# Kernel tuning notes

Measured on AMD Instinct MI355X. Metric: run time of the kernel, lower is better.

The kernel has to match this reference:

```python
import jax, jax.numpy as jnp
import numpy as np

CHUNK = 32  # config.scan_chunk_size


def setup_inputs() -> dict:
    key = jax.random.key(0)
    ks = jax.random.split(key, 12)
    B, T, D, SD, OD = 8, 2048, 512, 256, 64
    w = lambda i, shape: (jax.random.normal(ks[i], shape, dtype=jnp.float32) * 0.02)
    return {
        "x": jax.random.normal(ks[0], (B, T, D), dtype=jnp.float32),
        "gate_W": w(1, (D, SD)), "gate_b": jnp.zeros((SD,), jnp.float32),
        "in_W": w(2, (D, SD)), "in_b": jnp.zeros((SD,), jnp.float32),
        "out_W": w(3, (SD, D)), "out_b": jnp.zeros((D,), jnp.float32),
        "opv_W": w(4, (D, OD)), "opv_b": jnp.zeros((OD,), jnp.float32),
        "opk_W": w(5, (D, OD)), "opk_b": jnp.zeros((OD,), jnp.float32),
        "opq_W": w(6, (D, OD)), "opq_b": jnp.zeros((OD,), jnp.float32),
        "op_decay": jnp.full((OD,), 0.95, jnp.float32),
        "opout_W": w(7, (OD, D)), "opout_b": jnp.zeros((D,), jnp.float32),
        "ln_g": jnp.ones((D,), jnp.float32), "ln_b": jnp.zeros((D,), jnp.float32),
    }


def _chunked_scan(gates, drive, K):
    # gates, drive: [B,T,SD]; T divisible by K
    B, T, SD = drive.shape
    nC = T // K
    a = gates.reshape(B, nC, K, SD)
    b = drive.reshape(B, nC, K, SD)
    log_cum_a = jnp.cumsum(jnp.log(jnp.maximum(a, 1e-6)), axis=2)
    cum_a = jnp.exp(log_cum_a)                               # [B,nC,K,SD]
    cum_wb = jnp.cumsum(b / jnp.maximum(cum_a, 1e-8), axis=2)
    # sequential scan over chunks to propagate the carry h
    def step(h, inputs):
        ca_last, wb_last = inputs                            # [B,SD] each
        h_new = ca_last * (h + wb_last)
        return h_new, h                                      # emit h BEFORE this chunk
    h0 = jnp.zeros((B, SD), drive.dtype)
    _, h_prev = jax.lax.scan(
        step, h0,
        (cum_a[:, :, -1].transpose(1, 0, 2), cum_wb[:, :, -1].transpose(1, 0, 2)))
    h_prev = h_prev.transpose(1, 0, 2)                       # [B,nC,SD]
    states = cum_a * (h_prev[:, :, None, :] + cum_wb)
    return states.reshape(B, T, SD)


def _binding_scan_outer(v, k, q, decay):
    # v,k,q: [B,T,OD]; S_t = diag(decay) @ S_{t-1} + v_t k_t^T; o_t = S_t q_t
    B, T, OD = v.shape
    def step(S, vkq):
        vt, kt, qt = vkq                                     # [B,OD] each
        S_new = decay[None, :, None] * S + vt[:, :, None] * kt[:, None, :]
        o = jnp.einsum('bij,bj->bi', S_new, qt)
        return S_new, o
    S0 = jnp.zeros((B, OD, OD), v.dtype)
    _, outs = jax.lax.scan(step, S0, (v.transpose(1, 0, 2), k.transpose(1, 0, 2), q.transpose(1, 0, 2)))
    return outs.transpose(1, 0, 2)                           # [B,T,OD]


def reference(x, gate_W, gate_b, in_W, in_b, out_W, out_b,
              opv_W, opv_b, opk_W, opk_b, opq_W, opq_b, op_decay,
              opout_W, opout_b, ln_g, ln_b):
    gates = jax.nn.sigmoid(x @ gate_W + gate_b)              # [B,T,SD]
    drive = (1.0 - gates) * (x @ in_W + in_b)
    states = _chunked_scan(gates, drive, CHUNK)
    scan_out = states @ out_W + out_b                        # [B,T,D]
    # binding scan (mode='outer')
    v = x @ opv_W + opv_b
    k = x @ opk_W + opk_b
    q = x @ opq_W + opq_b
    dec = jax.nn.sigmoid(op_decay)
    bind = _binding_scan_outer(v, k, q, dec) @ opout_W + opout_b
    y = x + scan_out + bind
    mu = jnp.mean(y, axis=-1, keepdims=True)
    var = jnp.mean((y - mu) ** 2, axis=-1, keepdims=True)
    return (y - mu) / jnp.sqrt(var + 1e-5) * ln_g + ln_b
```

## Files before the change

kernel.cpp:

```cpp
#include <hip/hip_runtime.h>
#include <hip/hip_bf16.h>
#include <hip/hip_fp16.h>
#include <math.h>

#define BB 8
#define TT 2048
#define DD 512
#define SD 256
#define OD 64
#define CHUNK 32
#define NC 64
#define CB 64
#define NCB 32
#define MM (BB*TT)
#define KCAT 320

typedef __attribute__((ext_vector_type(8))) short bf16x8_t;
typedef __attribute__((ext_vector_type(4))) float f32x4;

__device__ __forceinline__ void gload_lds16(const void* gsrc, void* ldst) {
    __builtin_amdgcn_global_load_lds(
        (const __attribute__((address_space(1))) unsigned int*)gsrc,
        (__attribute__((address_space(3))) unsigned int*)ldst,
        16, 0, 0);
}

__device__ __forceinline__ float4 ldh4(const __half* p) {
    __half2 a = *(const __half2*)p;
    __half2 b = *(const __half2*)(p + 2);
    float2 fa = __half22float2(a), fb = __half22float2(b);
    return make_float4(fa.x, fa.y, fb.x, fb.y);
}

__global__ __launch_bounds__(256) void conv_w(
    const float* __restrict__ gate_W, const float* __restrict__ gate_b,
    const float* __restrict__ in_W,   const float* __restrict__ in_b,
    const float* __restrict__ opv_W,  const float* __restrict__ opk_W,
    const float* __restrict__ opq_W,
    const float* __restrict__ opv_b,  const float* __restrict__ opk_b,
    const float* __restrict__ opq_b,
    const float* __restrict__ out_W,  const float* __restrict__ out_b,
    const float* __restrict__ opout_W, const float* __restrict__ opout_b,
    __hip_bfloat16* __restrict__ Wcat,  __hip_bfloat16* __restrict__ Wcomb,
    float* __restrict__ bias_cat, float* __restrict__ bias_comb)
{
    int idx = blockIdx.x * 256 + threadIdx.x;
    if (idx < 393216) {
        int n = idx >> 9, k = idx & 511;
        float v;
        if (n < 256)       v = gate_W[k * 256 + n];
        else if (n < 512)  v = in_W[k * 256 + (n - 256)];
        else if (n < 704) {
            int h = (n - 512) >> 6, j = (n - 512) & 63;
            const float* W = (h == 0) ? opv_W : (h == 1) ? opk_W : opq_W;
            v = W[k * 64 + j];
        } else v = 0.f;
        Wcat[idx] = __float2bfloat16(v);
        return;
    }
    idx -= 393216;
    if (idx < 163840) {
        int n = idx / KCAT, k = idx % KCAT;
        float v = (k < 256) ? out_W[k * 512 + n] : opout_W[(k - 256) * 512 + n];
        Wcomb[idx] = __float2bfloat16(v);
        return;
    }
    idx -= 163840;
    if (idx < 768) {
        float v;
        if (idx < 256)      v = gate_b[idx];
        else if (idx < 512) v = in_b[idx - 256];
        else if (idx < 704) {
            int h = (idx - 512) >> 6, j = (idx - 512) & 63;
            v = (h == 0) ? opv_b[j] : (h == 1) ? opk_b[j] : opq_b[j];
        } else v = 0.f;
        bias_cat[idx] = v;
        return;
    }
    idx -= 768;
    if (idx < 512) bias_comb[idx] = out_b[idx] + opout_b[idx];
}

__global__ __launch_bounds__(512, 6) void gemm_proj(
    const float* __restrict__ A,
    const __hip_bfloat16* __restrict__ Bt,
    const float* __restrict__ bias,
    __half* __restrict__ out0,
    __half* __restrict__ out1,
    int M, int N, int K, int n0, int sigCols)
{
    constexpr int BM = 128, BK = 32;
    __shared__ alignas(16) __hip_bfloat16 Abuf[3][BM * BK];
    __shared__ alignas(16) __hip_bfloat16 Bbuf[3][BM * BK];
    const int tid = threadIdx.x;
    const int lane = tid & 63, wid = tid >> 6;
    const int wr = wid >> 2, wc = wid & 3;
    const int nbn = N >> 7;
    const int chunk = gridDim.x >> 3;
    const int b = blockIdx.x;
    const int orig = (b & 7) * chunk + (b >> 3);
    const int bm = (orig / nbn) * BM, bn = (orig % nbn) * BM;
    const int l15 = lane & 15, hgr = lane >> 4;

    const int grow = tid >> 2, gslot = tid & 3;
    const int gsw = gslot ^ ((grow >> 1) & 3);
    const float* srcA = A + (size_t)(bm + grow) * K + gslot * 8;
    const int wOffA = grow * 64 + gsw * 16;
    const __hip_bfloat16* srcB = Bt + (size_t)(bn + grow) * K + gsw * 8;
    const int ldsOffB = (tid & ~63) * 16;

    int offA[4], offB[2];
    #pragma unroll
    for (int mi = 0; mi < 4; ++mi) {
        int r = wr * 64 + mi * 16 + l15;
        offA[mi] = r * 64 + (hgr ^ ((r >> 1) & 3)) * 16;
    }
    #pragma unroll
    for (int nj = 0; nj < 2; ++nj) {
        int r = wc * 32 + nj * 16 + l15;
        offB[nj] = r * 64 + (hgr ^ ((r >> 1) & 3)) * 16;
    }

    f32x4 acc[4][2] = {};
    const int nk = K / BK;
    float4 pA0, pA1, qA0, qA1;

#define WRITE_A(IDX, R0, R1) do { \
        alignas(16) __hip_bfloat16 h_[8] = { \
            __float2bfloat16((R0).x), __float2bfloat16((R0).y), \
            __float2bfloat16((R0).z), __float2bfloat16((R0).w), \
            __float2bfloat16((R1).x), __float2bfloat16((R1).y), \
            __float2bfloat16((R1).z), __float2bfloat16((R1).w)}; \
        *(float4*)((char*)&Abuf[(IDX)][0] + wOffA) = *(float4*)h_; \
    } while (0)

#define FRAG_MFMA(T) do { \
        const char* ab_ = (const char*)&Abuf[(T) % 3][0]; \
        const char* bb_ = (const char*)&Bbuf[(T) % 3][0]; \
        bf16x8_t af_[4], bf_[2]; \
        _Pragma("unroll") \
        for (int mi = 0; mi < 4; ++mi) af_[mi] = *(const bf16x8_t*)(ab_ + offA[mi]); \
        _Pragma("unroll") \
        for (int nj = 0; nj < 2; ++nj) bf_[nj] = *(const bf16x8_t*)(bb_ + offB[nj]); \
        _Pragma("unroll") \
        for (int mi = 0; mi < 4; ++mi) \
            _Pragma("unroll") \
            for (int nj = 0; nj < 2; ++nj) \
                acc[mi][nj] = __builtin_amdgcn_mfma_f32_16x16x32_bf16( \
                    af_[mi], bf_[nj], acc[mi][nj], 0, 0, 0); \
    } while (0)

#define GEMM_STEP(T, I0, I1, W0, W1) do { \
        int k2_ = ((T) + 2) * BK; \
        I0 = *(const float4*)(srcA + k2_); \
        I1 = *(const float4*)(srcA + k2_ + 4); \
        gload_lds16(srcB + k2_, (char*)&Bbuf[((T) + 2) % 3][0] + ldsOffB); \
        FRAG_MFMA(T); \
        WRITE_A(((T) + 1) % 3, W0, W1); \
        asm volatile("s_waitcnt vmcnt(3) lgkmcnt(0)" ::: "memory"); \
        __builtin_amdgcn_sched_barrier(0); \
        __builtin_amdgcn_s_barrier(); \
        __builtin_amdgcn_sched_barrier(0); \
    } while (0)

    pA0 = *(const float4*)(srcA);
    pA1 = *(const float4*)(srcA + 4);
    gload_lds16(srcB, (char*)&Bbuf[0][0] + ldsOffB);
    qA0 = *(const float4*)(srcA + BK);
    qA1 = *(const float4*)(srcA + BK + 4);
    gload_lds16(srcB + BK, (char*)&Bbuf[1][0] + ldsOffB);
    asm volatile("s_waitcnt vmcnt(3)" ::: "memory");
    WRITE_A(0, pA0, pA1);
    asm volatile("s_waitcnt lgkmcnt(0)" ::: "memory");
    __builtin_amdgcn_sched_barrier(0);
    __builtin_amdgcn_s_barrier();
    __builtin_amdgcn_sched_barrier(0);

    for (int tt = 0; tt + 3 < nk; tt += 2) {
        GEMM_STEP(tt,     pA0, pA1, qA0, qA1);
        GEMM_STEP(tt + 1, qA0, qA1, pA0, pA1);
    }
    FRAG_MFMA(nk - 2);
    WRITE_A((nk - 1) % 3, qA0, qA1);
    __syncthreads();
    FRAG_MFMA(nk - 1);

#undef GEMM_STEP
#undef FRAG_MFMA
#undef WRITE_A

    const int n1 = N - n0;
    #pragma unroll
    for (int mi = 0; mi < 4; ++mi) {
        #pragma unroll
        for (int nj = 0; nj < 2; ++nj) {
            int col = bn + wc * 32 + nj * 16 + l15;
            int r0 = bm + wr * 64 + mi * 16 + hgr * 4;
            float bv = bias[col];
            #pragma unroll
            for (int e = 0; e < 4; ++e) {
                int row = r0 + e;
                float val = acc[mi][nj][e] + bv;
                if (col < n0) {
                    if (col < sigCols) val = 1.f / (1.f + expf(-val));
                    out0[(size_t)row * n0 + col] = __float2half(val);
                } else {
                    out1[(size_t)row * n1 + (col - n0)] = __float2half(val);
                }
            }
        }
    }
}

__device__ void scan_pass1_body(int blk,
    const __half* __restrict__ gi,
    float* __restrict__ ca_last, float* __restrict__ wb_last)
{
    int idx = blk * 256 + threadIdx.x;
    int sd = idx & 255;
    int c  = (idx >> 8) & 63;
    int b  = idx >> 14;
    size_t base = ((size_t)(b * TT + c * CHUNK)) * 512;
    float prod = 1.f, wb = 0.f;
    for (int i = 0; i < CHUNK; ++i) {
        size_t off = base + (size_t)i * 512;
        float g  = __half2float(gi[off + sd]);
        float il = __half2float(gi[off + 256 + sd]);
        float a = fmaxf(g, 1e-6f);
        prod *= a;
        wb += (1.f - g) * il / fmaxf(prod, 1e-8f);
    }
    int cidx = (b * NC + c) * SD + sd;
    ca_last[cidx] = prod;
    wb_last[cidx] = wb;
}

__device__ void scan_pass3_body(int blk,
    const __half* __restrict__ gi, const float* __restrict__ h_prev,
    __hip_bfloat16* __restrict__ cat)
{
    int idx = blk * 256 + threadIdx.x;
    int sd = idx & 255;
    int c  = (idx >> 8) & 63;
    int b  = idx >> 14;
    size_t base = ((size_t)(b * TT + c * CHUNK)) * 512;
    size_t obase = ((size_t)(b * TT + c * CHUNK)) * KCAT + sd;
    float h = h_prev[(b * NC + c) * SD + sd];
    float prod = 1.f, wb = 0.f;
    for (int i = 0; i < CHUNK; ++i) {
        size_t off = base + (size_t)i * 512;
        float g  = __half2float(gi[off + sd]);
        float il = __half2float(gi[off + 256 + sd]);
        float a = fmaxf(g, 1e-6f);
        prod *= a;
        wb += (1.f - g) * il / fmaxf(prod, 1e-8f);
        cat[obase + (size_t)i * KCAT] = __float2bfloat16(prod * (h + wb));
    }
}

#define LST 68
__device__ void bind_p1_body(int bc,
    const __half* __restrict__ vkq, const float* __restrict__ op_decay,
    float* __restrict__ o, float* __restrict__ dS,
    float* B1, float* B2, float* B3, float* l2d)
{
    const int b = bc >> 5, c = bc & 31;
    const size_t base = ((size_t)b * TT + (size_t)c * CB) * 256;
    const size_t obase = ((size_t)b * TT + (size_t)c * CB) * OD;
    const int tid = threadIdx.x;
    if (tid < 64) l2d[tid] = log2f(1.f / (1.f + expf(-op_decay[tid])));
    const int lr = tid >> 4, lc = (tid & 15) << 2;
    #pragma unroll
    for (int rr = 0; rr < 4; ++rr) {
        int t = lr + rr * 16;
        float4 qv = ldh4(&vkq[base + t * 256 + 128 + lc]);
        float4 kv = ldh4(&vkq[base + t * 256 + 64 + lc]);
        float q4[4] = {qv.x, qv.y, qv.z, qv.w};
        float k4[4] = {kv.x, kv.y, kv.z, kv.w};
        #pragma unroll
        for (int j = 0; j < 4; ++j) {
            B1[(lc + j) * LST + t] = q4[j];
            B2[(lc + j) * LST + t] = k4[j];
        }
    }
    __syncthreads();
    const int tx = tid & 15, ty = tid >> 4;
    {
        float a_acc[4][4] = {};
        for (int d = 0; d < 64; ++d) {
            float4 q4 = *(const float4*)&B1[d * LST + 4 * ty];
            float4 k4 = *(const float4*)&B2[d * LST + 4 * tx];
            float qr[4] = {q4.x, q4.y, q4.z, q4.w};
            float kr[4] = {k4.x, k4.y, k4.z, k4.w};
            #pragma unroll
            for (int r = 0; r < 4; ++r)
                #pragma unroll
                for (int s = 0; s < 4; ++s)
                    a_acc[r][s] = fmaf(qr[r], kr[s], a_acc[r][s]);
        }
        __syncthreads();
        #pragma unroll
        for (int s = 0; s < 4; ++s) {
            int ss = 4 * tx + s;
            float w[4];
            #pragma unroll
            for (int r = 0; r < 4; ++r)
                w[r] = (ss <= 4 * ty + r) ? a_acc[r][s] : 0.f;
            *(float4*)&B3[ss * LST + 4 * ty] = *(float4*)w;
        }
    }
    #pragma unroll
    for (int rr = 0; rr < 4; ++rr) {
        int m = lr + rr * 16;
        float4 vv = ldh4(&vkq[base + m * 256 + 0 + lc]);
        float4 kv = ldh4(&vkq[base + m * 256 + 64 + lc]);
        float v4[4] = {vv.x, vv.y, vv.z, vv.w};
        #pragma unroll
        for (int j = 0; j < 4; ++j)
            v4[j] *= exp2f(-(float)m * l2d[lc + j]);
        *(float4*)&B1[m * LST + lc] = *(float4*)v4;
        float k4[4] = {kv.x, kv.y, kv.z, kv.w};
        *(float4*)&B2[m * LST + lc] = *(float4*)k4;
    }
    __syncthreads();
    {
        float p[4][4] = {};
        for (int s = 0; s < 64; ++s) {
            float4 a4 = *(const float4*)&B3[s * LST + 4 * ty];
            float4 v4 = *(const float4*)&B1[s * LST + 4 * tx];
            float ar[4] = {a4.x, a4.y, a4.z, a4.w};
            float vr[4] = {v4.x, v4.y, v4.z, v4.w};
            #pragma unroll
            for (int r = 0; r < 4; ++r)
                #pragma unroll
                for (int i2 = 0; i2 < 4; ++i2)
                    p[r][i2] = fmaf(ar[r], vr[i2], p[r][i2]);
        }
        #pragma unroll
        for (int r = 0; r < 4; ++r) {
            int t = 4 * ty + r;
            float w[4];
            #pragma unroll
            for (int i2 = 0; i2 < 4; ++i2)
                w[i2] = exp2f((float)t * l2d[4 * tx + i2]) * p[r][i2];
            *(float4*)&o[obase + t * OD + 4 * tx] = *(float4*)w;
        }
    }
    {
        float sacc[4][4] = {};
        for (int m = 0; m < 64; ++m) {
            float4 v4 = *(const float4*)&B1[m * LST + 4 * ty];
            float4 k4 = *(const float4*)&B2[m * LST + 4 * tx];
            float vr[4] = {v4.x, v4.y, v4.z, v4.w};
            float kr[4] = {k4.x, k4.y, k4.z, k4.w};
            #pragma unroll
            for (int r = 0; r < 4; ++r)
                #pragma unroll
                for (int j = 0; j < 4; ++j)
                    sacc[r][j] = fmaf(vr[r], kr[j], sacc[r][j]);
        }
        float* dSb = dS + (size_t)bc * 4096;
        #pragma unroll
        for (int r = 0; r < 4; ++r) {
            int i = 4 * ty + r;
            float scale = exp2f(63.f * l2d[i]);
            float w[4];
            #pragma unroll
            for (int j2 = 0; j2 < 4; ++j2)
                w[j2] = scale * sacc[r][j2];
            *(float4*)&dSb[i * 64 + 4 * tx] = *(float4*)w;
        }
    }
}

__device__ void bind_p3_body(int bc,
    const __half* __restrict__ vkq, const float* __restrict__ Sstart,
    const float* __restrict__ op_decay, const float* __restrict__ o,
    __hip_bfloat16* __restrict__ cat,
    float* B1, float* B2, float* l2d)
{
    const int b = bc >> 5, c = bc & 31;
    const size_t base = ((size_t)b * TT + (size_t)c * CB) * 256;
    const size_t obase = ((size_t)b * TT + (size_t)c * CB) * OD;
    const size_t cbase = ((size_t)b * TT + (size_t)c * CB) * KCAT + 256;
    const int tid = threadIdx.x;
    if (tid < 64) l2d[tid] = log2f(1.f / (1.f + expf(-op_decay[tid])));
    const int lr = tid >> 4, lc = (tid & 15) << 2;
    const float* Sb = Sstart + (size_t)bc * 4096;
    #pragma unroll
    for (int rr = 0; rr < 4; ++rr) {
        int t = lr + rr * 16;
        float4 qv = ldh4(&vkq[base + t * 256 + 128 + lc]);
        float4 sv = *(const float4*)&Sb[t * 64 + lc];
        float q4[4] = {qv.x, qv.y, qv.z, qv.w};
        float s4[4] = {sv.x, sv.y, sv.z, sv.w};
        #pragma unroll
        for (int j = 0; j < 4; ++j) {
            B1[(lc + j) * LST + t] = q4[j];
            B2[(lc + j) * LST + t] = s4[j];
        }
    }
    __syncthreads();
    const int tx = tid & 15, ty = tid >> 4;
    float acc[4][4] = {};
    for (int j = 0; j < 64; ++j) {
        float4 q4 = *(const float4*)&B1[j * LST + 4 * ty];
        float4 s4 = *(const float4*)&B2[j * LST + 4 * tx];
        float qr[4] = {q4.x, q4.y, q4.z, q4.w};
        float sr[4] = {s4.x, s4.y, s4.z, s4.w};
        #pragma unroll
        for (int r = 0; r < 4; ++r)
            #pragma unroll
            for (int i2 = 0; i2 < 4; ++i2)
                acc[r][i2] = fmaf(qr[r], sr[i2], acc[r][i2]);
    }
    #pragma unroll
    for (int r = 0; r < 4; ++r) {
        int l = 4 * ty + r;
        alignas(8) __hip_bfloat16 w[4];
        #pragma unroll
        for (int i2 = 0; i2 < 4; ++i2) {
            int i = 4 * tx + i2;
            float val = o[obase + l * OD + i] + exp2f((float)(l + 1) * l2d[i]) * acc[r][i2];
            w[i2] = __float2bfloat16(val);
        }
        *(float2*)&cat[cbase + l * KCAT + 4 * tx] = *(float2*)w;
    }
}

__global__ __launch_bounds__(256) void fused1(
    const __half* __restrict__ gi, const __half* __restrict__ vkq,
    const float* __restrict__ op_decay,
    float* __restrict__ ca_last, float* __restrict__ wb_last,
    float* __restrict__ o_intra, float* __restrict__ dS)
{
    __shared__ float B1[64 * LST];
    __shared__ float B2[64 * LST];
    __shared__ float B3[64 * LST];
    __shared__ float l2d[64];
    const int bid = blockIdx.x;
    if (bid < 256) bind_p1_body(bid, vkq, op_decay, o_intra, dS, B1, B2, B3, l2d);
    else           scan_pass1_body(bid - 256, gi, ca_last, wb_last);
}

__global__ __launch_bounds__(256) void fused2(
    const float* __restrict__ dS, const float* __restrict__ op_decay,
    float* __restrict__ Sstart,
    const float* __restrict__ ca_last, const float* __restrict__ wb_last,
    float* __restrict__ h_prev)
{
    const int bid = blockIdx.x;
    if (bid < 128) {
        int idx = bid * 256 + threadIdx.x;
        int j = idx & 63, i = (idx >> 6) & 63, b = idx >> 12;
        float dec = 1.f / (1.f + expf(-op_decay[i]));
        float d64 = exp2f(64.f * log2f(dec));
        float S = 0.f;
        for (int c = 0; c < NCB; ++c) {
            size_t o = (((size_t)b * NCB + c) * 4096) + i * 64 + j;
            Sstart[o] = S;
            S = d64 * S + dS[o];
        }
    } else {
        int idx = (bid - 128) * 256 + threadIdx.x;
        int sd = idx & 255;
        int b  = idx >> 8;
        float h = 0.f;
        for (int c = 0; c < NC; ++c) {
            int o = (b * NC + c) * SD + sd;
            h_prev[o] = h;
            h = ca_last[o] * (h + wb_last[o]);
        }
    }
}

__global__ __launch_bounds__(256) void fused3(
    const __half* __restrict__ gi, const float* __restrict__ h_prev,
    const __half* __restrict__ vkq, const float* __restrict__ Sstart,
    const float* __restrict__ op_decay, const float* __restrict__ o_intra,
    __hip_bfloat16* __restrict__ cat)
{
    __shared__ float B1[64 * LST];
    __shared__ float B2[64 * LST];
    __shared__ float l2d[64];
    const int bid = blockIdx.x;
    if (bid < 256) bind_p3_body(bid, vkq, Sstart, op_decay, o_intra, cat, B1, B2, l2d);
    else           scan_pass3_body(bid - 256, gi, h_prev, cat);
}

__global__ __launch_bounds__(512) void outgemm_ln(
    const __hip_bfloat16* __restrict__ cat,
    const __hip_bfloat16* __restrict__ Wcomb,
    const float* __restrict__ bias_comb,
    const float* __restrict__ x,
    const float* __restrict__ lng, const float* __restrict__ lnb,
    float* __restrict__ y)
{
    constexpr int BM = 32, BK = 32, NN = 512;
    __shared__ alignas(16) __hip_bfloat16 As[2][BM * BK];
    __shared__ alignas(16) __hip_bfloat16 Bs[2][NN * BK];
    __shared__ float psum[8][BM], psum2[8][BM], mvmu[BM], mvrs[BM];
    const int tid = threadIdx.x;
    const int lane = tid & 63, wid = tid >> 6;
    const int l15 = lane & 15, hgr = lane >> 4;
    const int bm = blockIdx.x * BM;

    const __hip_bfloat16* srcA = cat;
    int ldsOffA = 0;
    {
        int gg = (wid & 1) * 64 + lane;
        int row = gg >> 2, sl = (gg & 3) ^ ((row >> 1) & 3);
        srcA = cat + (size_t)(bm + row) * KCAT + sl * 8;
        ldsOffA = (wid & 1) * 1024;
    }
    const __hip_bfloat16* srcB[4];
    int ldsOffB[4];
    #pragma unroll
    for (int c = 0; c < 4; ++c) {
        int gg = (wid * 4 + c) * 64 + lane;
        int row = gg >> 2, sl = (gg & 3) ^ ((row >> 1) & 3);
        srcB[c] = Wcomb + (size_t)row * KCAT + sl * 8;
        ldsOffB[c] = (wid * 4 + c) * 1024;
    }
    int offA[2], offB[4];
    #pragma unroll
    for (int mi = 0; mi < 2; ++mi) {
        int r = mi * 16 + l15;
        offA[mi] = r * 64 + (hgr ^ ((r >> 1) & 3)) * 16;
    }
    #pragma unroll
    for (int nj = 0; nj < 4; ++nj) {
        int n = wid * 64 + nj * 16 + l15;
        offB[nj] = n * 64 + (hgr ^ ((n >> 1) & 3)) * 16;
    }

    f32x4 acc[2][4] = {};
    constexpr int nk = KCAT / BK;

    if (wid < 2) gload_lds16(srcA, (char*)&As[0][0] + ldsOffA);
    #pragma unroll
    for (int c = 0; c < 4; ++c) gload_lds16(srcB[c], (char*)&Bs[0][0] + ldsOffB[c]);
    __syncthreads();

    int cur = 0;
    for (int t = 0; t < nk; ++t) {
        if (t + 1 < nk) {
            int k0 = (t + 1) * BK;
            if (wid < 2) gload_lds16(srcA + k0, (char*)&As[cur ^ 1][0] + ldsOffA);
            #pragma unroll
            for (int c = 0; c < 4; ++c)
                gload_lds16(srcB[c] + k0, (char*)&Bs[cur ^ 1][0] + ldsOffB[c]);
        }
        bf16x8_t af[2], bfr[4];
        #pragma unroll
        for (int mi = 0; mi < 2; ++mi)
            af[mi] = *(const bf16x8_t*)((const char*)&As[cur][0] + offA[mi]);
        #pragma unroll
        for (int nj = 0; nj < 4; ++nj)
            bfr[nj] = *(const bf16x8_t*)((const char*)&Bs[cur][0] + offB[nj]);
        #pragma unroll
        for (int mi = 0; mi < 2; ++mi)
            #pragma unroll
            for (int nj = 0; nj < 4; ++nj)
                acc[mi][nj] = __builtin_amdgcn_mfma_f32_16x16x32_bf16(
                    af[mi], bfr[nj], acc[mi][nj], 0, 0, 0);
        __syncthreads();
        cur ^= 1;
    }

    #pragma unroll
    for (int nj = 0; nj < 4; ++nj) {
        int col = wid * 64 + nj * 16 + l15;
        float bc_ = bias_comb[col];
        #pragma unroll
        for (int mi = 0; mi < 2; ++mi) {
            int r0 = bm + mi * 16 + hgr * 4;
            #pragma unroll
            for (int e = 0; e < 4; ++e)
                acc[mi][nj][e] += bc_ + x[(size_t)(r0 + e) * DD + col];
        }
    }
    float s[8], s2[8];
    #pragma unroll
    for (int mi = 0; mi < 2; ++mi)
        #pragma unroll
        for (int e = 0; e < 4; ++e) {
            float a = 0.f, b2 = 0.f;
            #pragma unroll
            for (int nj = 0; nj < 4; ++nj) {
                float v = acc[mi][nj][e];
                a += v; b2 += v * v;
            }
            s[mi * 4 + e] = a; s2[mi * 4 + e] = b2;
        }
    #pragma unroll
    for (int off = 1; off <= 8; off <<= 1)
        #pragma unroll
        for (int i = 0; i < 8; ++i) {
            s[i]  += __shfl_xor(s[i], off);
            s2[i] += __shfl_xor(s2[i], off);
        }
    if (l15 == 0) {
        #pragma unroll
        for (int mi = 0; mi < 2; ++mi)
            #pragma unroll
            for (int e = 0; e < 4; ++e) {
                int lr = mi * 16 + hgr * 4 + e;
                psum[wid][lr]  = s[mi * 4 + e];
                psum2[wid][lr] = s2[mi * 4 + e];
            }
    }
    __syncthreads();
    if (tid < BM) {
        float tot = 0.f, tot2 = 0.f;
        #pragma unroll
        for (int w2 = 0; w2 < 8; ++w2) { tot += psum[w2][tid]; tot2 += psum2[w2][tid]; }
        float mu = tot * (1.f / 512.f);
        float var = tot2 * (1.f / 512.f) - mu * mu;
        mvmu[tid] = mu;
        mvrs[tid] = rsqrtf(var + 1e-5f);
    }
    __syncthreads();
    #pragma unroll
    for (int nj = 0; nj < 4; ++nj) {
        int col = wid * 64 + nj * 16 + l15;
        float g = lng[col], bb = lnb[col];
        #pragma unroll
        for (int mi = 0; mi < 2; ++mi) {
            #pragma unroll
            for (int e = 0; e < 4; ++e) {
                int lr = mi * 16 + hgr * 4 + e;
                y[(size_t)(bm + lr) * DD + col] =
                    (acc[mi][nj][e] - mvmu[lr]) * mvrs[lr] * g + bb;
            }
        }
    }
}

extern "C" void kernel_launch(void* const* d_in, const int* in_sizes, int n_in,
                              void* d_out, int out_size, void* d_ws, size_t ws_size,
                              hipStream_t stream)
{
    const float* x       = (const float*)d_in[0];
    const float* gate_W  = (const float*)d_in[1];
    const float* gate_b  = (const float*)d_in[2];
    const float* in_W    = (const float*)d_in[3];
    const float* in_b    = (const float*)d_in[4];
    const float* out_W   = (const float*)d_in[5];
    const float* out_b   = (const float*)d_in[6];
    const float* opv_W   = (const float*)d_in[7];
    const float* opv_b   = (const float*)d_in[8];
    const float* opk_W   = (const float*)d_in[9];
    const float* opk_b   = (const float*)d_in[10];
    const float* opq_W   = (const float*)d_in[11];
    const float* opq_b   = (const float*)d_in[12];
    const float* op_dec  = (const float*)d_in[13];
    const float* opout_W = (const float*)d_in[14];
    const float* opout_b = (const float*)d_in[15];
    const float* ln_g    = (const float*)d_in[16];
    const float* ln_b    = (const float*)d_in[17];
    float* y = (float*)d_out;

    char* w = (char*)d_ws;
    auto alloc = [&](size_t bytes) { char* p = w; w += (bytes + 255) & ~(size_t)255; return p; };
    __half* gi       = (__half*)alloc((size_t)MM * 512 * 2);
    __half* vkq      = (__half*)alloc((size_t)MM * 256 * 2);
    float* o_intra   = (float*)alloc((size_t)MM * 64 * 4);
    float* ca_last   = (float*)alloc((size_t)BB * NC * SD * 4);
    float* wb_last   = (float*)alloc((size_t)BB * NC * SD * 4);
    float* h_prev    = (float*)alloc((size_t)BB * NC * SD * 4);
    float* dS        = (float*)alloc((size_t)BB * NCB * 4096 * 4);
    float* Sstart    = (float*)alloc((size_t)BB * NCB * 4096 * 4);
    float* bias_cat  = (float*)alloc(768 * 4);
    float* bias_comb = (float*)alloc(512 * 4);
    __hip_bfloat16* cat   = (__hip_bfloat16*)alloc((size_t)MM * KCAT * 2);
    __hip_bfloat16* Wcat  = (__hip_bfloat16*)alloc((size_t)768 * 512 * 2);
    __hip_bfloat16* Wcomb = (__hip_bfloat16*)alloc((size_t)512 * KCAT * 2);

    hipLaunchKernelGGL(conv_w, dim3((393216 + 163840 + 768 + 512 + 255) / 256), dim3(256), 0, stream,
                       gate_W, gate_b, in_W, in_b, opv_W, opk_W, opq_W,
                       opv_b, opk_b, opq_b, out_W, out_b, opout_W, opout_b,
                       Wcat, Wcomb, bias_cat, bias_comb);
    hipLaunchKernelGGL(gemm_proj, dim3(6 * (MM / 128)), dim3(512), 0, stream,
                       x, Wcat, bias_cat, gi, vkq,
                       MM, 768, 512, 512, 256);
    hipLaunchKernelGGL(fused1, dim3(768), dim3(256), 0, stream,
                       gi, vkq, op_dec, ca_last, wb_last, o_intra, dS);
    hipLaunchKernelGGL(fused2, dim3(136), dim3(256), 0, stream,
                       dS, op_dec, Sstart, ca_last, wb_last, h_prev);
    hipLaunchKernelGGL(fused3, dim3(768), dim3(256), 0, stream,
                       gi, h_prev, vkq, Sstart, op_dec, o_intra, cat);
    hipLaunchKernelGGL(outgemm_ln, dim3(MM / 32), dim3(512), 0, stream,
                       cat, Wcomb, bias_comb, x, ln_g, ln_b, y);
}
```

Measured before the change: 87.36 us.

## Double the projection GEMM K-tile to 64 with wider swizzle and fewer barriers

Raises the projection GEMM's K tile from 32 to 64. Each thread now issues two A loads and two B LDS loads per stage, the XOR swizzle widens to 8 slots, and the A buffer goes from triple to double buffering. MFMA bursts are wrapped in s_setprio. This halves the number of K iterations and barriers per tile. In exchange, LDS use and register pressure rise and the occupancy hint drops from 6 to 4 blocks.

```diff
diff --git a/kernel.cpp b/kernel.cpp
--- a/kernel.cpp
+++ b/kernel.cpp
@@ -81,7 +81,7 @@
     if (idx < 512) bias_comb[idx] = out_b[idx] + opout_b[idx];
 }
 
-__global__ __launch_bounds__(512, 6) void gemm_proj(
+__global__ __launch_bounds__(512, 4) void gemm_proj(
     const float* __restrict__ A,
     const __hip_bfloat16* __restrict__ Bt,
     const float* __restrict__ bias,
@@ -89,8 +89,8 @@
     __half* __restrict__ out1,
     int M, int N, int K, int n0, int sigCols)
 {
-    constexpr int BM = 128, BK = 32;
-    __shared__ alignas(16) __hip_bfloat16 Abuf[3][BM * BK];
+    constexpr int BM = 128, BK = 64;
+    __shared__ alignas(16) __hip_bfloat16 Abuf[2][BM * BK];
     __shared__ alignas(16) __hip_bfloat16 Bbuf[3][BM * BK];
     const int tid = threadIdx.x;
     const int lane = tid & 63, wid = tid >> 6;
@@ -102,88 +102,121 @@
     const int bm = (orig / nbn) * BM, bn = (orig % nbn) * BM;
     const int l15 = lane & 15, hgr = lane >> 4;
 
-    const int grow = tid >> 2, gslot = tid & 3;
-    const int gsw = gslot ^ ((grow >> 1) & 3);
-    const float* srcA = A + (size_t)(bm + grow) * K + gslot * 8;
-    const int wOffA = grow * 64 + gsw * 16;
-    const __hip_bfloat16* srcB = Bt + (size_t)(bn + grow) * K + gsw * 8;
-    const int ldsOffB = (tid & ~63) * 16;
-
-    int offA[4], offB[2];
+    const float* srcA[2];
+    int wOffA[2];
+    const __hip_bfloat16* srcB[2];
+    int ldsOffB[2];
+    #pragma unroll
+    for (int s = 0; s < 2; ++s) {
+        int ga = s * 512 + tid;
+        int row = ga >> 3, sl = ga & 7;
+        int sw = sl ^ ((row >> 1) & 7);
+        srcA[s] = A + (size_t)(bm + row) * K + sl * 8;
+        wOffA[s] = row * 128 + sw * 16;
+        srcB[s] = Bt + (size_t)(bn + row) * K + sw * 8;
+        ldsOffB[s] = (s * 512 + (tid & ~63)) * 16;
+    }
+    int offA[4][2], offB[2][2];
     #pragma unroll
     for (int mi = 0; mi < 4; ++mi) {
         int r = wr * 64 + mi * 16 + l15;
-        offA[mi] = r * 64 + (hgr ^ ((r >> 1) & 3)) * 16;
+        #pragma unroll
+        for (int h = 0; h < 2; ++h)
+            offA[mi][h] = r * 128 + (((h * 4 + hgr) ^ ((r >> 1) & 7)) * 16);
     }
     #pragma unroll
     for (int nj = 0; nj < 2; ++nj) {
         int r = wc * 32 + nj * 16 + l15;
-        offB[nj] = r * 64 + (hgr ^ ((r >> 1) & 3)) * 16;
+        #pragma unroll
+        for (int h = 0; h < 2; ++h)
+            offB[nj][h] = r * 128 + (((h * 4 + hgr) ^ ((r >> 1) & 7)) * 16);
     }
 
     f32x4 acc[4][2] = {};
     const int nk = K / BK;
-    float4 pA0, pA1, qA0, qA1;
-
-#define WRITE_A(IDX, R0, R1) do { \
-        alignas(16) __hip_bfloat16 h_[8] = { \
-            __float2bfloat16((R0).x), __float2bfloat16((R0).y), \
-            __float2bfloat16((R0).z), __float2bfloat16((R0).w), \
-            __float2bfloat16((R1).x), __float2bfloat16((R1).y), \
-            __float2bfloat16((R1).z), __float2bfloat16((R1).w)}; \
-        *(float4*)((char*)&Abuf[(IDX)][0] + wOffA) = *(float4*)h_; \
+    float4 pA[4], qA[4];
+
+#define WRITE_A(IDX, R) do { \
+        _Pragma("unroll") \
+        for (int s_ = 0; s_ < 2; ++s_) { \
+            alignas(16) __hip_bfloat16 h_[8] = { \
+                __float2bfloat16(R[2*s_].x), __float2bfloat16(R[2*s_].y), \
+                __float2bfloat16(R[2*s_].z), __float2bfloat16(R[2*s_].w), \
+                __float2bfloat16(R[2*s_+1].x), __float2bfloat16(R[2*s_+1].y), \
+                __float2bfloat16(R[2*s_+1].z), __float2bfloat16(R[2*s_+1].w)}; \
+            *(float4*)((char*)&Abuf[(IDX)][0] + wOffA[s_]) = *(float4*)h_; \
+        } \
     } while (0)
 
-#define FRAG_MFMA(T) do { \
-        const char* ab_ = (const char*)&Abuf[(T) % 3][0]; \
-        const char* bb_ = (const char*)&Bbuf[(T) % 3][0]; \
-        bf16x8_t af_[4], bf_[2]; \
-        _Pragma("unroll") \
-        for (int mi = 0; mi < 4; ++mi) af_[mi] = *(const bf16x8_t*)(ab_ + offA[mi]); \
-        _Pragma("unroll") \
-        for (int nj = 0; nj < 2; ++nj) bf_[nj] = *(const bf16x8_t*)(bb_ + offB[nj]); \
+#define FRAG_MFMA(AI, BI) do { \
+        const char* ab_ = (const char*)&Abuf[(AI)][0]; \
+        const char* bb_ = (const char*)&Bbuf[(BI)][0]; \
+        bf16x8_t af_[4][2], bf_[2][2]; \
         _Pragma("unroll") \
         for (int mi = 0; mi < 4; ++mi) \
             _Pragma("unroll") \
-            for (int nj = 0; nj < 2; ++nj) \
-                acc[mi][nj] = __builtin_amdgcn_mfma_f32_16x16x32_bf16( \
-                    af_[mi], bf_[nj], acc[mi][nj], 0, 0, 0); \
+            for (int h = 0; h < 2; ++h) \
+                af_[mi][h] = *(const bf16x8_t*)(ab_ + offA[mi][h]); \
+        _Pragma("unroll") \
+        for (int nj = 0; nj < 2; ++nj) \
+            _Pragma("unroll") \
+            for (int h = 0; h < 2; ++h) \
+                bf_[nj][h] = *(const bf16x8_t*)(bb_ + offB[nj][h]); \
+        __builtin_amdgcn_s_setprio(1); \
+        _Pragma("unroll") \
+        for (int h = 0; h < 2; ++h) \
+            _Pragma("unroll") \
+            for (int mi = 0; mi < 4; ++mi) \
+                _Pragma("unroll") \
+                for (int nj = 0; nj < 2; ++nj) \
+                    acc[mi][nj] = __builtin_amdgcn_mfma_f32_16x16x32_bf16( \
+                        af_[mi][h], bf_[nj][h], acc[mi][nj], 0, 0, 0); \
+        __builtin_amdgcn_s_setprio(0); \
     } while (0)
 
-#define GEMM_STEP(T, I0, I1, W0, W1) do { \
+#define GEMM_STEP(T, I, W) do { \
         int k2_ = ((T) + 2) * BK; \
-        I0 = *(const float4*)(srcA + k2_); \
-        I1 = *(const float4*)(srcA + k2_ + 4); \
-        gload_lds16(srcB + k2_, (char*)&Bbuf[((T) + 2) % 3][0] + ldsOffB); \
-        FRAG_MFMA(T); \
-        WRITE_A(((T) + 1) % 3, W0, W1); \
-        asm volatile("s_waitcnt vmcnt(3) lgkmcnt(0)" ::: "memory"); \
+        I[0] = *(const float4*)(srcA[0] + k2_); \
+        I[1] = *(const float4*)(srcA[0] + k2_ + 4); \
+        I[2] = *(const float4*)(srcA[1] + k2_); \
+        I[3] = *(const float4*)(srcA[1] + k2_ + 4); \
+        gload_lds16(srcB[0] + k2_, (char*)&Bbuf[((T) + 2) % 3][0] + ldsOffB[0]); \
+        gload_lds16(srcB[1] + k2_, (char*)&Bbuf[((T) + 2) % 3][0] + ldsOffB[1]); \
+        FRAG_MFMA((T) & 1, (T) % 3); \
+        WRITE_A(((T) + 1) & 1, W); \
+        asm volatile("s_waitcnt vmcnt(6) lgkmcnt(0)" ::: "memory"); \
         __builtin_amdgcn_sched_barrier(0); \
         __builtin_amdgcn_s_barrier(); \
         __builtin_amdgcn_sched_barrier(0); \
     } while (0)
 
-    pA0 = *(const float4*)(srcA);
-    pA1 = *(const float4*)(srcA + 4);
-    gload_lds16(srcB, (char*)&Bbuf[0][0] + ldsOffB);
-    qA0 = *(const float4*)(srcA + BK);
-    qA1 = *(const float4*)(srcA + BK + 4);
-    gload_lds16(srcB + BK, (char*)&Bbuf[1][0] + ldsOffB);
-    asm volatile("s_waitcnt vmcnt(3)" ::: "memory");
-    WRITE_A(0, pA0, pA1);
+    pA[0] = *(const float4*)(srcA[0]);
+    pA[1] = *(const float4*)(srcA[0] + 4);
+    pA[2] = *(const float4*)(srcA[1]);
+    pA[3] = *(const float4*)(srcA[1] + 4);
+    gload_lds16(srcB[0], (char*)&Bbuf[0][0] + ldsOffB[0]);
+    gload_lds16(srcB[1], (char*)&Bbuf[0][0] + ldsOffB[1]);
+    qA[0] = *(const float4*)(srcA[0] + BK);
+    qA[1] = *(const float4*)(srcA[0] + BK + 4);
+    qA[2] = *(const float4*)(srcA[1] + BK);
+    qA[3] = *(const float4*)(srcA[1] + BK + 4);
+    gload_lds16(srcB[0] + BK, (char*)&Bbuf[1][0] + ldsOffB[0]);
+    gload_lds16(srcB[1] + BK, (char*)&Bbuf[1][0] + ldsOffB[1]);
+    asm volatile("s_waitcnt vmcnt(6)" ::: "memory");
+    WRITE_A(0, pA);
     asm volatile("s_waitcnt lgkmcnt(0)" ::: "memory");
     __builtin_amdgcn_sched_barrier(0);
     __builtin_amdgcn_s_barrier();
     __builtin_amdgcn_sched_barrier(0);
 
     for (int tt = 0; tt + 3 < nk; tt += 2) {
-        GEMM_STEP(tt,     pA0, pA1, qA0, qA1);
-        GEMM_STEP(tt + 1, qA0, qA1, pA0, pA1);
-    }
-    FRAG_MFMA(nk - 2);
-    WRITE_A((nk - 1) % 3, qA0, qA1);
+        GEMM_STEP(tt,     pA, qA);
+        GEMM_STEP(tt + 1, qA, pA);
+    }
+    FRAG_MFMA((nk - 2) & 1, (nk - 2) % 3);
+    WRITE_A((nk - 1) & 1, qA);
     __syncthreads();
-    FRAG_MFMA(nk - 1);
+    FRAG_MFMA((nk - 1) & 1, (nk - 1) % 3);
 
 #undef GEMM_STEP
 #undef FRAG_MFMA
```

Result: slower. 118.9 us (+36.1%).

## Fold inter-chunk carry scans into pass3 by recomputing prefixes per block

Applied to the files above, without the earlier changes.

Removes the separate fused2 kernel that computed chunk-start carries (h_prev and Sstart) sequentially. Each pass3 block now recomputes its own carry by walking all earlier chunk summaries (ca_last/wb_last or dS). This drops one kernel launch, a grid-wide dependency and the intermediate buffers. In exchange it adds redundant work that grows with chunk index, quadratic in the number of chunks, and makes later blocks read more dS data.

```diff
diff --git a/kernel.cpp b/kernel.cpp
--- a/kernel.cpp
+++ b/kernel.cpp
@@ -236,16 +236,21 @@
 }
 
 __device__ void scan_pass3_body(int blk,
-    const __half* __restrict__ gi, const float* __restrict__ h_prev,
+    const __half* __restrict__ gi,
+    const float* __restrict__ ca_last, const float* __restrict__ wb_last,
     __hip_bfloat16* __restrict__ cat)
 {
     int idx = blk * 256 + threadIdx.x;
     int sd = idx & 255;
     int c  = (idx >> 8) & 63;
     int b  = idx >> 14;
+    float h = 0.f;
+    for (int cc = 0; cc < c; ++cc) {
+        int o = (b * NC + cc) * SD + sd;
+        h = ca_last[o] * (h + wb_last[o]);
+    }
     size_t base = ((size_t)(b * TT + c * CHUNK)) * 512;
     size_t obase = ((size_t)(b * TT + c * CHUNK)) * KCAT + sd;
-    float h = h_prev[(b * NC + c) * SD + sd];
     float prod = 1.f, wb = 0.f;
     for (int i = 0; i < CHUNK; ++i) {
         size_t off = base + (size_t)i * 512;
@@ -374,7 +379,7 @@
 }
 
 __device__ void bind_p3_body(int bc,
-    const __half* __restrict__ vkq, const float* __restrict__ Sstart,
+    const __half* __restrict__ vkq, const float* __restrict__ dS,
     const float* __restrict__ op_decay, const float* __restrict__ o,
     __hip_bfloat16* __restrict__ cat,
     float* B1, float* B2, float* l2d)
@@ -385,15 +390,24 @@
     const size_t cbase = ((size_t)b * TT + (size_t)c * CB) * KCAT + 256;
     const int tid = threadIdx.x;
     if (tid < 64) l2d[tid] = log2f(1.f / (1.f + expf(-op_decay[tid])));
+    __syncthreads();
     const int lr = tid >> 4, lc = (tid & 15) << 2;
-    const float* Sb = Sstart + (size_t)bc * 4096;
     #pragma unroll
     for (int rr = 0; rr < 4; ++rr) {
         int t = lr + rr * 16;
         float4 qv = ldh4(&vkq[base + t * 256 + 128 + lc]);
-        float4 sv = *(const float4*)&Sb[t * 64 + lc];
+        float d64 = exp2f(64.f * l2d[t]);
+        float s0 = 0.f, s1 = 0.f, s2 = 0.f, s3 = 0.f;
+        for (int cc = 0; cc < c; ++cc) {
+            const float* dSb = dS + (((size_t)(b * NCB + cc)) * 4096) + t * 64 + lc;
+            float4 dv = *(const float4*)dSb;
+            s0 = d64 * s0 + dv.x;
+            s1 = d64 * s1 + dv.y;
+            s2 = d64 * s2 + dv.z;
+            s3 = d64 * s3 + dv.w;
+        }
         float q4[4] = {qv.x, qv.y, qv.z, qv.w};
-        float s4[4] = {sv.x, sv.y, sv.z, sv.w};
+        float s4[4] = {s0, s1, s2, s3};
         #pragma unroll
         for (int j = 0; j < 4; ++j) {
             B1[(lc + j) * LST + t] = q4[j];
@@ -443,40 +457,10 @@
     else           scan_pass1_body(bid - 256, gi, ca_last, wb_last);
 }
 
-__global__ __launch_bounds__(256) void fused2(
-    const float* __restrict__ dS, const float* __restrict__ op_decay,
-    float* __restrict__ Sstart,
+__global__ __launch_bounds__(256) void fused3(
+    const __half* __restrict__ gi,
     const float* __restrict__ ca_last, const float* __restrict__ wb_last,
-    float* __restrict__ h_prev)
-{
-    const int bid = blockIdx.x;
-    if (bid < 128) {
-        int idx = bid * 256 + threadIdx.x;
-        int j = idx & 63, i = (idx >> 6) & 63, b = idx >> 12;
-        float dec = 1.f / (1.f + expf(-op_decay[i]));
-        float d64 = exp2f(64.f * log2f(dec));
-        float S = 0.f;
-        for (int c = 0; c < NCB; ++c) {
-            size_t o = (((size_t)b * NCB + c) * 4096) + i * 64 + j;
-            Sstart[o] = S;
-            S = d64 * S + dS[o];
-        }
-    } else {
-        int idx = (bid - 128) * 256 + threadIdx.x;
-        int sd = idx & 255;
-        int b  = idx >> 8;
-        float h = 0.f;
-        for (int c = 0; c < NC; ++c) {
-            int o = (b * NC + c) * SD + sd;
-            h_prev[o] = h;
-            h = ca_last[o] * (h + wb_last[o]);
-        }
-    }
-}
-
-__global__ __launch_bounds__(256) void fused3(
-    const __half* __restrict__ gi, const float* __restrict__ h_prev,
-    const __half* __restrict__ vkq, const float* __restrict__ Sstart,
+    const __half* __restrict__ vkq, const float* __restrict__ dS,
     const float* __restrict__ op_decay, const float* __restrict__ o_intra,
     __hip_bfloat16* __restrict__ cat)
 {
@@ -484,8 +468,8 @@
     __shared__ float B2[64 * LST];
     __shared__ float l2d[64];
     const int bid = blockIdx.x;
-    if (bid < 256) bind_p3_body(bid, vkq, Sstart, op_decay, o_intra, cat, B1, B2, l2d);
-    else           scan_pass3_body(bid - 256, gi, h_prev, cat);
+    if (bid < 256) bind_p3_body(bid, vkq, dS, op_decay, o_intra, cat, B1, B2, l2d);
+    else           scan_pass3_body(bid - 256, gi, ca_last, wb_last, cat);
 }
 
 __global__ __launch_bounds__(512) void outgemm_ln(
@@ -668,9 +652,7 @@
     float* o_intra   = (float*)alloc((size_t)MM * 64 * 4);
     float* ca_last   = (float*)alloc((size_t)BB * NC * SD * 4);
     float* wb_last   = (float*)alloc((size_t)BB * NC * SD * 4);
-    float* h_prev    = (float*)alloc((size_t)BB * NC * SD * 4);
     float* dS        = (float*)alloc((size_t)BB * NCB * 4096 * 4);
-    float* Sstart    = (float*)alloc((size_t)BB * NCB * 4096 * 4);
     float* bias_cat  = (float*)alloc(768 * 4);
     float* bias_comb = (float*)alloc(512 * 4);
     __hip_bfloat16* cat   = (__hip_bfloat16*)alloc((size_t)MM * KCAT * 2);
@@ -686,10 +668,8 @@
                        MM, 768, 512, 512, 256);
     hipLaunchKernelGGL(fused1, dim3(768), dim3(256), 0, stream,
                        gi, vkq, op_dec, ca_last, wb_last, o_intra, dS);
-    hipLaunchKernelGGL(fused2, dim3(136), dim3(256), 0, stream,
-                       dS, op_dec, Sstart, ca_last, wb_last, h_prev);
     hipLaunchKernelGGL(fused3, dim3(768), dim3(256), 0, stream,
-                       gi, h_prev, vkq, Sstart, op_dec, o_intra, cat);
+                       gi, ca_last, wb_last, vkq, dS, op_dec, o_intra, cat);
     hipLaunchKernelGGL(outgemm_ln, dim3(MM / 32), dim3(512), 0, stream,
                        cat, Wcomb, bias_comb, x, ln_g, ln_b, y);
 }
```

After: 104.2 us. 19.2% more time.
